# Optimization experiments

Hardware: AMD Instinct MI355X
Metric: run time of the kernel (lower is better)

Reference implementation:

```python
import jax, jax.numpy as jnp
import numpy as np

SCALE = 0.08838834764831845  # 1/sqrt(128)
SOFT_CAP = 0.0
NUM_KV_HEADS = 8
RANK = 0


def setup_inputs() -> dict:
    key = jax.random.key(0)
    k0, k1, k2, k3 = jax.random.split(key, 4)
    B, H, D = 16, 32, 128
    T = 4096            # max kv length (pages per seq, page_size=1)
    P = B * T           # total pages
    q = jax.random.normal(k0, (B, H, D), jnp.float32)
    k_cache = jax.random.normal(k1, (P, 1, NUM_KV_HEADS, D), jnp.float32)
    v_cache = jax.random.normal(k2, (P, 1, NUM_KV_HEADS, D), jnp.float32)
    global_kv_lens = jax.random.randint(k3, (1, B), 1, T + 1).astype(jnp.int32)
    block_table = jnp.arange(B * T, dtype=jnp.int32).reshape(B, T)
    return {"q": q, "k_cache": k_cache, "v_cache": v_cache,
            "global_kv_lens": global_kv_lens, "block_table": block_table}


def reference(q, k_cache, v_cache, global_kv_lens, block_table):
    # Paged GQA flash-decode attention; num_ranks=1 so the Iris cross-rank
    # combine is the identity and the split-KV online softmax equals a
    # single stable softmax over the full (masked) KV length.
    kv_lens = global_kv_lens[RANK]                  # [B]
    k = k_cache[block_table, 0]                     # [B, T, KVH, D] paged gather
    v = v_cache[block_table, 0]                     # [B, T, KVH, D]
    B, H, D = q.shape
    G = H // NUM_KV_HEADS
    qh = q.reshape(B, NUM_KV_HEADS, G, D)
    s = jnp.einsum('bkgd,btkd->bkgt', qh, k) * SCALE  # [B, KVH, G, T]
    if SOFT_CAP > 0:
        s = SOFT_CAP * jnp.tanh(s / SOFT_CAP)
    T = k.shape[1]
    valid = jnp.arange(T)[None, :] < kv_lens[:, None]            # [B, T]
    s = jnp.where(valid[:, None, None, :], s, -jnp.inf)
    p = jax.nn.softmax(s, axis=-1)
    out = jnp.einsum('bkgt,btkd->bkgd', p, v).reshape(B, H, D)
    return out
```

## Files before the change

kernel.cpp:

```cpp
#include <hip/hip_runtime.h>
#include <cstdint>
#include <cstddef>


#define NB 16
#define NH 32
#define HD 128
#define NT 4096
#define NKVH 8
#define NG 4
#define NSPLIT 16
#define CHUNK (NT / NSPLIT)
#define TILE_T 16
#define NWAVE 4
#define ROW 132
#define PART_STRIDE 520
#define SCALE_F 0.08838834764831845f

__device__ __forceinline__ void wave_sync() {
    __builtin_amdgcn_wave_barrier();
    __asm__ volatile("" ::: "memory");
}

__global__ __launch_bounds__(256) void attn_partial_kernel(
    const float* __restrict__ q,
    const float* __restrict__ kc,
    const float* __restrict__ vc,
    const int*   __restrict__ kv_lens,
    const int*   __restrict__ btab,
    float*       __restrict__ part)
{
    __shared__ float q_lds[NG][ROW];
    __shared__ float kv_lds[NWAVE][TILE_T][ROW];
    __shared__ float p_lds[NWAVE][TILE_T][NG];
    __shared__ float a_lds[NWAVE][NG];
    __shared__ float ml_lds[NWAVE][NG][2];

    const int bid = blockIdx.x;
    const int c   = bid % NSPLIT;
    const int kvh = (bid / NSPLIT) % NKVH;
    const int b   = bid / (NSPLIT * NKVH);
    const int tid  = threadIdx.x;
    const int w    = tid >> 6;
    const int lane = tid & 63;

    const int kv_len = kv_lens[b];
    const int t0c = c * CHUNK;
    const int t1c = min(t0c + CHUNK, kv_len);

    float* pb = part + (size_t)bid * PART_STRIDE;

    if (t0c >= kv_len) {
        for (int i = tid; i < PART_STRIDE; i += 256)
            pb[i] = (i >= 512 && i < 516) ? -1e30f : 0.0f;
        return;
    }

    {
        int g  = tid >> 6;
        int dd = (tid & 63) * 2;
        const float* qp = q + ((size_t)(b * NH + kvh * NG + g)) * HD + dd;
        q_lds[g][dd]     = qp[0];
        q_lds[g][dd + 1] = qp[1];
    }
    __syncthreads();

    float m_g = -1e30f;
    float l_g = 0.0f;
    float o00=0,o01=0,o10=0,o11=0,o20=0,o21=0,o30=0,o31=0;

    const int half = lane >> 5;
    const int d4   = lane & 31;
    const int tt_s = lane >> 2;
    const int g_s  = lane & 3;
    const int dp   = lane * 2;

    for (int t0 = t0c + w * TILE_T; t0 < t1c; t0 += NWAVE * TILE_T) {
        int pg = 0;
        if (lane < TILE_T) {
            int t = t0 + lane;
            pg = btab[b * NT + ((t < t1c) ? t : t0)];
        }

        float4 vreg[8];
        #pragma unroll
        for (int r = 0; r < 8; ++r) {
            int tt = r * 2 + half;
            int page = __shfl(pg, tt);
            const float4 kk = *((const float4*)(kc + (size_t)page * (NKVH * HD) + kvh * HD) + d4);
            *(float4*)&kv_lds[w][tt][d4 * 4] = kk;
        }
        #pragma unroll
        for (int r = 0; r < 8; ++r) {
            int tt = r * 2 + half;
            int page = __shfl(pg, tt);
            vreg[r] = *((const float4*)(vc + (size_t)page * (NKVH * HD) + kvh * HD) + d4);
        }
        wave_sync();

        float s = 0.0f;
        #pragma unroll
        for (int i = 0; i < 32; ++i) {
            float4 kk = *(const float4*)&kv_lds[w][tt_s][i * 4];
            float4 qq = *(const float4*)&q_lds[g_s][i * 4];
            s = fmaf(kk.x, qq.x, s);
            s = fmaf(kk.y, qq.y, s);
            s = fmaf(kk.z, qq.z, s);
            s = fmaf(kk.w, qq.w, s);
        }
        s *= SCALE_F;
        if (t0 + tt_s >= t1c) s = -1e30f;

        float tmax = s;
        #pragma unroll
        for (int off = 4; off < 64; off <<= 1)
            tmax = fmaxf(tmax, __shfl_xor(tmax, off));
        float m_new = fmaxf(m_g, tmax);
        float alpha = __expf(m_g - m_new);
        float p     = __expf(s - m_new);
        float tsum = p;
        #pragma unroll
        for (int off = 4; off < 64; off <<= 1)
            tsum += __shfl_xor(tsum, off);
        l_g = l_g * alpha + tsum;
        m_g = m_new;

        p_lds[w][tt_s][g_s] = p;
        if (tt_s == 0) a_lds[w][g_s] = alpha;
        wave_sync();

        #pragma unroll
        for (int r = 0; r < 8; ++r) {
            int tt = r * 2 + half;
            *(float4*)&kv_lds[w][tt][d4 * 4] = vreg[r];
        }
        wave_sync();

        float a0 = a_lds[w][0], a1 = a_lds[w][1], a2 = a_lds[w][2], a3 = a_lds[w][3];
        o00 *= a0; o01 *= a0; o10 *= a1; o11 *= a1;
        o20 *= a2; o21 *= a2; o30 *= a3; o31 *= a3;
        #pragma unroll
        for (int t = 0; t < TILE_T; ++t) {
            float2 vv = *(const float2*)&kv_lds[w][t][dp];
            float4 pp = *(const float4*)&p_lds[w][t][0];
            o00 = fmaf(pp.x, vv.x, o00); o01 = fmaf(pp.x, vv.y, o01);
            o10 = fmaf(pp.y, vv.x, o10); o11 = fmaf(pp.y, vv.y, o11);
            o20 = fmaf(pp.z, vv.x, o20); o21 = fmaf(pp.z, vv.y, o21);
            o30 = fmaf(pp.w, vv.x, o30); o31 = fmaf(pp.w, vv.y, o31);
        }
        wave_sync();
    }

    {
        float* ow = &kv_lds[w][0][0];
        ow[0 * HD + dp] = o00; ow[0 * HD + dp + 1] = o01;
        ow[1 * HD + dp] = o10; ow[1 * HD + dp + 1] = o11;
        ow[2 * HD + dp] = o20; ow[2 * HD + dp + 1] = o21;
        ow[3 * HD + dp] = o30; ow[3 * HD + dp + 1] = o31;
        if (tt_s == 0) { ml_lds[w][g_s][0] = m_g; ml_lds[w][g_s][1] = l_g; }
    }
    __syncthreads();

    {
        int g  = tid >> 6;
        int d2 = (tid & 63) * 2;
        float M = fmaxf(fmaxf(ml_lds[0][g][0], ml_lds[1][g][0]),
                        fmaxf(ml_lds[2][g][0], ml_lds[3][g][0]));
        float L = 0.0f, O0 = 0.0f, O1 = 0.0f;
        #pragma unroll
        for (int wv = 0; wv < NWAVE; ++wv) {
            float sc = __expf(ml_lds[wv][g][0] - M);
            L  += ml_lds[wv][g][1] * sc;
            const float* owv = &kv_lds[wv][0][0];
            O0 += owv[g * HD + d2]     * sc;
            O1 += owv[g * HD + d2 + 1] * sc;
        }
        pb[g * HD + d2]     = O0;
        pb[g * HD + d2 + 1] = O1;
        if ((tid & 63) == 0) { pb[512 + g] = M; pb[516 + g] = L; }
    }
}

__global__ __launch_bounds__(256) void attn_combine_kernel(
    const float* __restrict__ part, float* __restrict__ out)
{
    const int bid = blockIdx.x;
    const int tid = threadIdx.x;
    const int g  = tid >> 6;
    const int d2 = (tid & 63) * 2;
    const int b   = bid / NKVH;
    const int kvh = bid % NKVH;
    const float* pb = part + (size_t)bid * NSPLIT * PART_STRIDE;

    float M = -1e30f;
    #pragma unroll
    for (int cc = 0; cc < NSPLIT; ++cc)
        M = fmaxf(M, pb[cc * PART_STRIDE + 512 + g]);
    float L = 0.0f, O0 = 0.0f, O1 = 0.0f;
    #pragma unroll
    for (int cc = 0; cc < NSPLIT; ++cc) {
        float mc = pb[cc * PART_STRIDE + 512 + g];
        float sc = __expf(mc - M);
        L  += pb[cc * PART_STRIDE + 516 + g] * sc;
        O0 += pb[cc * PART_STRIDE + g * HD + d2]     * sc;
        O1 += pb[cc * PART_STRIDE + g * HD + d2 + 1] * sc;
    }
    float inv = 1.0f / L;
    const int h = kvh * NG + g;
    out[((size_t)b * NH + h) * HD + d2]     = O0 * inv;
    out[((size_t)b * NH + h) * HD + d2 + 1] = O1 * inv;
}

extern "C" void kernel_launch(void* const* d_in, const int* in_sizes, int n_in,
                              void* d_out, int out_size, void* d_ws, size_t ws_size,
                              hipStream_t stream)
{
    const float* q   = (const float*)d_in[0];
    const float* kc  = (const float*)d_in[1];
    const float* vc  = (const float*)d_in[2];
    const int*   kvl = (const int*)d_in[3];
    const int*   bt  = (const int*)d_in[4];
    float* part = (float*)d_ws;

    attn_partial_kernel<<<NB * NKVH * NSPLIT, 256, 0, stream>>>(q, kc, vc, kvl, bt, part);
    attn_combine_kernel<<<NB * NKVH, 256, 0, stream>>>(part, (float*)d_out);
}
```

Baseline: 497.9 us.

## Prefetch next K tile into registers and split QK dot across lanes

Loads the next tile's K rows into registers while the current tile is computed, so global-load latency overlaps with compute. The QK dot product now has each lane handle one token and one 32-element quarter of the head dim for all four query heads, combining the partial sums with cross-lane shuffles. The softmax scale is folded into Q when Q is loaded, and per-lane page lookups replace the shuffled block-table value. This raises register pressure (extra float4 arrays for K) and adds shuffle reductions, which could lower occupancy.

```diff
diff --git a/kernel.cpp b/kernel.cpp
--- a/kernel.cpp
+++ b/kernel.cpp
@@ -60,80 +60,100 @@
         int g  = tid >> 6;
         int dd = (tid & 63) * 2;
         const float* qp = q + ((size_t)(b * NH + kvh * NG + g)) * HD + dd;
-        q_lds[g][dd]     = qp[0];
-        q_lds[g][dd + 1] = qp[1];
+        q_lds[g][dd]     = qp[0] * SCALE_F;
+        q_lds[g][dd + 1] = qp[1] * SCALE_F;
     }
     __syncthreads();
+
+    const int half = lane >> 5;
+    const int d4   = lane & 31;
+    const int t_s  = lane & 15;
+    const int seg  = lane >> 4;
+    const int dp   = lane * 2;
+
+    const float* kbase = kc + (size_t)kvh * HD;
+    const float* vbase = vc + (size_t)kvh * HD;
+    const int*   bt_b  = btab + b * NT;
 
     float m_g = -1e30f;
     float l_g = 0.0f;
     float o00=0,o01=0,o10=0,o11=0,o20=0,o21=0,o30=0,o31=0;
 
-    const int half = lane >> 5;
-    const int d4   = lane & 31;
-    const int tt_s = lane >> 2;
-    const int g_s  = lane & 3;
-    const int dp   = lane * 2;
-
-    for (int t0 = t0c + w * TILE_T; t0 < t1c; t0 += NWAVE * TILE_T) {
-        int pg = 0;
-        if (lane < TILE_T) {
-            int t = t0 + lane;
-            pg = btab[b * NT + ((t < t1c) ? t : t0)];
-        }
-
-        float4 vreg[8];
+    float4 ka[8], kb_[8], vv[8];
+
+    int t0 = t0c + w * TILE_T;
+    if (t0 < t1c) {
         #pragma unroll
         for (int r = 0; r < 8; ++r) {
-            int tt = r * 2 + half;
-            int page = __shfl(pg, tt);
-            const float4 kk = *((const float4*)(kc + (size_t)page * (NKVH * HD) + kvh * HD) + d4);
-            *(float4*)&kv_lds[w][tt][d4 * 4] = kk;
-        }
+            int t = t0 + r * 2 + half;
+            int page = bt_b[(t < t1c) ? t : t0c];
+            ka[r] = *((const float4*)(kbase + (size_t)page * (NKVH * HD)) + d4);
+        }
+    }
+
+    for (; t0 < t1c; t0 += NWAVE * TILE_T) {
         #pragma unroll
         for (int r = 0; r < 8; ++r) {
-            int tt = r * 2 + half;
-            int page = __shfl(pg, tt);
-            vreg[r] = *((const float4*)(vc + (size_t)page * (NKVH * HD) + kvh * HD) + d4);
-        }
-        wave_sync();
-
-        float s = 0.0f;
-        #pragma unroll
-        for (int i = 0; i < 32; ++i) {
-            float4 kk = *(const float4*)&kv_lds[w][tt_s][i * 4];
-            float4 qq = *(const float4*)&q_lds[g_s][i * 4];
-            s = fmaf(kk.x, qq.x, s);
-            s = fmaf(kk.y, qq.y, s);
-            s = fmaf(kk.z, qq.z, s);
-            s = fmaf(kk.w, qq.w, s);
-        }
-        s *= SCALE_F;
-        if (t0 + tt_s >= t1c) s = -1e30f;
+            int t = t0 + r * 2 + half;
+            int page = bt_b[(t < t1c) ? t : t0c];
+            vv[r] = *((const float4*)(vbase + (size_t)page * (NKVH * HD)) + d4);
+        }
+        #pragma unroll
+        for (int r = 0; r < 8; ++r)
+            *(float4*)&kv_lds[w][r * 2 + half][d4 * 4] = ka[r];
+
+        const int t0n = t0 + NWAVE * TILE_T;
+        if (t0n < t1c) {
+            #pragma unroll
+            for (int r = 0; r < 8; ++r) {
+                int t = t0n + r * 2 + half;
+                int page = bt_b[(t < t1c) ? t : t0c];
+                kb_[r] = *((const float4*)(kbase + (size_t)page * (NKVH * HD)) + d4);
+            }
+        }
+        wave_sync();
+
+        float s0=0,s1=0,s2=0,s3=0;
+        #pragma unroll
+        for (int i = 0; i < 8; ++i) {
+            float4 kk = *(const float4*)&kv_lds[w][t_s][seg * 32 + i * 4];
+            float4 q0 = *(const float4*)&q_lds[0][seg * 32 + i * 4];
+            float4 q1 = *(const float4*)&q_lds[1][seg * 32 + i * 4];
+            float4 q2 = *(const float4*)&q_lds[2][seg * 32 + i * 4];
+            float4 q3 = *(const float4*)&q_lds[3][seg * 32 + i * 4];
+            s0 = fmaf(kk.x,q0.x,fmaf(kk.y,q0.y,fmaf(kk.z,q0.z,fmaf(kk.w,q0.w,s0))));
+            s1 = fmaf(kk.x,q1.x,fmaf(kk.y,q1.y,fmaf(kk.z,q1.z,fmaf(kk.w,q1.w,s1))));
+            s2 = fmaf(kk.x,q2.x,fmaf(kk.y,q2.y,fmaf(kk.z,q2.z,fmaf(kk.w,q2.w,s2))));
+            s3 = fmaf(kk.x,q3.x,fmaf(kk.y,q3.y,fmaf(kk.z,q3.z,fmaf(kk.w,q3.w,s3))));
+        }
+        s0 += __shfl_xor(s0, 16); s0 += __shfl_xor(s0, 32);
+        s1 += __shfl_xor(s1, 16); s1 += __shfl_xor(s1, 32);
+        s2 += __shfl_xor(s2, 16); s2 += __shfl_xor(s2, 32);
+        s3 += __shfl_xor(s3, 16); s3 += __shfl_xor(s3, 32);
+        float s = (seg == 0) ? s0 : (seg == 1) ? s1 : (seg == 2) ? s2 : s3;
+        if (t0 + t_s >= t1c) s = -1e30f;
 
         float tmax = s;
         #pragma unroll
-        for (int off = 4; off < 64; off <<= 1)
+        for (int off = 1; off < 16; off <<= 1)
             tmax = fmaxf(tmax, __shfl_xor(tmax, off));
         float m_new = fmaxf(m_g, tmax);
         float alpha = __expf(m_g - m_new);
         float p     = __expf(s - m_new);
         float tsum = p;
         #pragma unroll
-        for (int off = 4; off < 64; off <<= 1)
+        for (int off = 1; off < 16; off <<= 1)
             tsum += __shfl_xor(tsum, off);
         l_g = l_g * alpha + tsum;
         m_g = m_new;
 
-        p_lds[w][tt_s][g_s] = p;
-        if (tt_s == 0) a_lds[w][g_s] = alpha;
-        wave_sync();
-
-        #pragma unroll
-        for (int r = 0; r < 8; ++r) {
-            int tt = r * 2 + half;
-            *(float4*)&kv_lds[w][tt][d4 * 4] = vreg[r];
-        }
+        p_lds[w][t_s][seg] = p;
+        if (t_s == 0) a_lds[w][seg] = alpha;
+        wave_sync();
+
+        #pragma unroll
+        for (int r = 0; r < 8; ++r)
+            *(float4*)&kv_lds[w][r * 2 + half][d4 * 4] = vv[r];
         wave_sync();
 
         float a0 = a_lds[w][0], a1 = a_lds[w][1], a2 = a_lds[w][2], a3 = a_lds[w][3];
@@ -141,14 +161,17 @@
         o20 *= a2; o21 *= a2; o30 *= a3; o31 *= a3;
         #pragma unroll
         for (int t = 0; t < TILE_T; ++t) {
-            float2 vv = *(const float2*)&kv_lds[w][t][dp];
-            float4 pp = *(const float4*)&p_lds[w][t][0];
-            o00 = fmaf(pp.x, vv.x, o00); o01 = fmaf(pp.x, vv.y, o01);
-            o10 = fmaf(pp.y, vv.x, o10); o11 = fmaf(pp.y, vv.y, o11);
-            o20 = fmaf(pp.z, vv.x, o20); o21 = fmaf(pp.z, vv.y, o21);
-            o30 = fmaf(pp.w, vv.x, o30); o31 = fmaf(pp.w, vv.y, o31);
-        }
-        wave_sync();
+            float2 vvv = *(const float2*)&kv_lds[w][t][dp];
+            float4 pp  = *(const float4*)&p_lds[w][t][0];
+            o00 = fmaf(pp.x, vvv.x, o00); o01 = fmaf(pp.x, vvv.y, o01);
+            o10 = fmaf(pp.y, vvv.x, o10); o11 = fmaf(pp.y, vvv.y, o11);
+            o20 = fmaf(pp.z, vvv.x, o20); o21 = fmaf(pp.z, vvv.y, o21);
+            o30 = fmaf(pp.w, vvv.x, o30); o31 = fmaf(pp.w, vvv.y, o31);
+        }
+        wave_sync();
+
+        #pragma unroll
+        for (int r = 0; r < 8; ++r) ka[r] = kb_[r];
     }
 
     {
@@ -157,7 +180,7 @@
         ow[1 * HD + dp] = o10; ow[1 * HD + dp + 1] = o11;
         ow[2 * HD + dp] = o20; ow[2 * HD + dp + 1] = o21;
         ow[3 * HD + dp] = o30; ow[3 * HD + dp + 1] = o31;
-        if (tt_s == 0) { ml_lds[w][g_s][0] = m_g; ml_lds[w][g_s][1] = l_g; }
+        if (t_s == 0) { ml_lds[w][seg][0] = m_g; ml_lds[w][seg][1] = l_g; }
     }
     __syncthreads();
 
```

New measurement: 574.9 us. 15.5% more time.
